# Kernel tuning notes

Hardware: AMD Instinct MI355X
Metric: run time of the kernel (lower is better)

The kernel has to match this reference:

```python
import jax, jax.numpy as jnp
import numpy as np

B, L, S = 1, 2048, 2048
D_MODEL, H = 1024, 16
DK = D_MODEL // H  # d_keys = d_values = 64


def sparsemax(z):
    # sparsemax along last axis: proj of z onto the simplex
    K = z.shape[-1]
    z_sorted = jnp.flip(jnp.sort(z, axis=-1), axis=-1)
    cs = jnp.cumsum(z_sorted, axis=-1)
    r = jnp.arange(1, K + 1, dtype=z.dtype)
    support = 1.0 + r * z_sorted > cs
    k = jnp.sum(support, axis=-1, keepdims=True)
    tau = (jnp.take_along_axis(cs, k.astype(jnp.int32) - 1, axis=-1) - 1.0) / k.astype(z.dtype)
    return jnp.maximum(z - tau, 0.0)


def setup_inputs() -> dict:
    key = jax.random.key(0)
    ks = jax.random.split(key, 12)
    sc = 1.0 / np.sqrt(D_MODEL)
    return {
        "queries": jax.random.normal(ks[0], (B, L, D_MODEL), jnp.float32),
        "keys": jax.random.normal(ks[1], (B, S, D_MODEL), jnp.float32),
        "values": jax.random.normal(ks[2], (B, S, D_MODEL), jnp.float32),
        "Wq": jax.random.normal(ks[3], (D_MODEL, H * DK), jnp.float32) * sc,
        "bq": jnp.zeros((H * DK,), jnp.float32),
        "Wk": jax.random.normal(ks[4], (D_MODEL, H * DK), jnp.float32) * sc,
        "bk": jnp.zeros((H * DK,), jnp.float32),
        "Wv": jax.random.normal(ks[5], (H * DK, H * DK), jnp.float32) * sc,
        "bv": jnp.zeros((H * DK,), jnp.float32),
        "Wo": jax.random.normal(ks[6], (H * DK, D_MODEL), jnp.float32) * sc,
        "bo": jnp.zeros((D_MODEL,), jnp.float32),
    }


def reference(queries, keys, values, Wq, bq, Wk, bk, Wv, bv, Wo, bo):
    # projections (note: input `values` is unused, matching the torch source)
    q = (queries @ Wq + bq).reshape(B, L, H, DK)
    k_flat = keys @ Wk + bk                      # [B,S,H*DK]
    k = k_flat.reshape(B, S, H, DK)
    v = (k_flat @ Wv + bv).reshape(B, S, H, DK)  # value_projection(key_projection(keys))
    scale = 1.0 / np.sqrt(DK)
    scores = jnp.einsum('blhe,bshe->bhls', q, k) * scale  # [B,H,L,S]
    A = sparsemax(scores)
    out = jnp.einsum('bhls,bshd->blhd', A, v)             # [B,L,H,DK]
    # mix=True: transpose(2,1) -> [B,H,L,D] then view(B,L,-1)
    out = jnp.swapaxes(out, 1, 2).reshape(B, L, H * DK)
    return out @ Wo + bo
```

## Files before the change

### kernel.cpp

```cpp
#include <hip/hip_runtime.h>
#include <hip/hip_bf16.h>


typedef __attribute__((ext_vector_type(8))) short short8;
typedef __attribute__((ext_vector_type(4))) float floatx4;

#define SRC_BF16 0
#define SRC_F32  1
#define SRC_RT   2
#define CAP 128

__device__ __forceinline__ short f2bf(float f) {
    __hip_bfloat16 h = __float2bfloat16(f);
    return *reinterpret_cast<const short*>(&h);
}
__device__ __forceinline__ unsigned short f2bfu(float f) {
    __hip_bfloat16 h = __float2bfloat16(f);
    return *reinterpret_cast<const unsigned short*>(&h);
}
__device__ __forceinline__ float bf2f(unsigned short u) {
    return __uint_as_float(((unsigned)u) << 16);
}
__device__ __forceinline__ unsigned fmap(float f) {
    unsigned u = __float_as_uint(f);
    return (u & 0x80000000u) ? ~u : (u | 0x80000000u);
}
__device__ __forceinline__ float funmap(unsigned u) {
    return (u & 0x80000000u) ? __uint_as_float(u ^ 0x80000000u) : __uint_as_float(~u);
}

__global__ void detect_k(const short* __restrict__ q, int n, int* __restrict__ flag)
{
    const int tid = threadIdx.x;
    int bad = 0;
    for (int i = tid; i < n; i += 64) {
        float f = bf2f((unsigned short)q[i]);
        if (!(fabsf(f) < 1e10f)) bad = 1;
    }
    unsigned long long m = __ballot(bad != 0);
    if (tid == 0) *flag = (m != 0ULL) ? 1 : 0;
}

__global__ __launch_bounds__(256)
void convert2_k(const void* __restrict__ s0, const void* __restrict__ s1,
                short* __restrict__ d0, short* __restrict__ d1,
                const int* __restrict__ dflag)
{
    const void* s = blockIdx.z ? s1 : s0;
    short* d = blockIdx.z ? d1 : d0;
    const size_t i = ((size_t)blockIdx.x * 256 + threadIdx.x) * 8;
    short8 o;
    if (*dflag) {
        const float4 f0 = ((const float4*)((const float*)s + i))[0];
        const float4 f1 = ((const float4*)((const float*)s + i))[1];
        o[0] = f2bf(f0.x); o[1] = f2bf(f0.y); o[2] = f2bf(f0.z); o[3] = f2bf(f0.w);
        o[4] = f2bf(f1.x); o[5] = f2bf(f1.y); o[6] = f2bf(f1.z); o[7] = f2bf(f1.w);
    } else {
        o = *(const short8*)((const short*)s + i);
    }
    *(short8*)(d + i) = o;
}

struct TP4 {
    const void* s[4];
    short* d[4];
};
__global__ __launch_bounds__(256)
void transpose4_k(TP4 p, int R, int C, const int* __restrict__ dflag)
{
    __shared__ short T[64][72];
    const int tid = threadIdx.x;
    const int bC = blockIdx.x, bR = blockIdx.y;
    const void* src = p.s[blockIdx.z];
    short* dst = p.d[blockIdx.z];
    const bool f32 = (*dflag != 0);

    const int colg = (tid & 7) * 8;
    #pragma unroll
    for (int h = 0; h < 2; ++h) {
        const int row = (tid >> 3) + 32 * h;
        const size_t idx = (size_t)(bR * 64 + row) * (size_t)C + (size_t)(bC * 64 + colg);
        short e[8];
        if (f32) {
            const float4 f0 = ((const float4*)((const float*)src + idx))[0];
            const float4 f1 = ((const float4*)((const float*)src + idx))[1];
            e[0] = f2bf(f0.x); e[1] = f2bf(f0.y); e[2] = f2bf(f0.z); e[3] = f2bf(f0.w);
            e[4] = f2bf(f1.x); e[5] = f2bf(f1.y); e[6] = f2bf(f1.z); e[7] = f2bf(f1.w);
        } else {
            short8 s = *(const short8*)((const short*)src + idx);
            #pragma unroll
            for (int j = 0; j < 8; ++j) e[j] = s[j];
        }
        #pragma unroll
        for (int j = 0; j < 8; ++j) T[colg + j][row] = e[j];
    }
    __syncthreads();
    #pragma unroll
    for (int h = 0; h < 2; ++h) {
        const int orow = (tid >> 3) + 32 * h;
        const int ocolg = (tid & 7) * 8;
        const size_t idx = (size_t)(bC * 64 + orow) * (size_t)R + (size_t)(bR * 64 + ocolg);
        *(short8*)(dst + idx) = *(const short8*)&T[orow][ocolg];
    }
}

struct GJ { const short* A; const short* B; const void* bias; void* C; };

template<int OSRC>
__global__ __launch_bounds__(256)
void gemm64_bt_k(GJ j0, GJ j1, const int* __restrict__ dflag)
{
    __shared__ __align__(16) short As[64][40];
    __shared__ __align__(16) short Bs[64][40];

    const GJ j = blockIdx.z ? j1 : j0;
    const int rtf = *dflag;

    const int tid  = threadIdx.x;
    const int bN   = blockIdx.x, bM = blockIdx.y;
    const int lane = tid & 63, wave = tid >> 6;
    const int wm   = (wave >> 1) * 32;
    const int wn   = (wave & 1) * 32;
    const int quad = lane >> 4, r16 = lane & 15;

    floatx4 acc[2][2];
    #pragma unroll
    for (int i = 0; i < 2; ++i)
        #pragma unroll
        for (int jj = 0; jj < 2; ++jj)
            acc[i][jj] = (floatx4){0.f, 0.f, 0.f, 0.f};

    const int ar = tid >> 2, ac = (tid & 3) * 8;

    for (int k0 = 0; k0 < 1024; k0 += 32) {
        *(short8*)&As[ar][ac] =
            *(const short8*)(j.A + (size_t)(bM * 64 + ar) * 1024 + (size_t)(k0 + ac));
        *(short8*)&Bs[ar][ac] =
            *(const short8*)(j.B + (size_t)(bN * 64 + ar) * 1024 + (size_t)(k0 + ac));
        __syncthreads();

        short8 a0 = *(const short8*)&As[wm + r16][quad * 8];
        short8 a1 = *(const short8*)&As[wm + 16 + r16][quad * 8];
        short8 b0 = *(const short8*)&Bs[wn + r16][quad * 8];
        short8 b1 = *(const short8*)&Bs[wn + 16 + r16][quad * 8];

        acc[0][0] = __builtin_amdgcn_mfma_f32_16x16x32_bf16(a0, b0, acc[0][0], 0, 0, 0);
        acc[0][1] = __builtin_amdgcn_mfma_f32_16x16x32_bf16(a0, b1, acc[0][1], 0, 0, 0);
        acc[1][0] = __builtin_amdgcn_mfma_f32_16x16x32_bf16(a1, b0, acc[1][0], 0, 0, 0);
        acc[1][1] = __builtin_amdgcn_mfma_f32_16x16x32_bf16(a1, b1, acc[1][1], 0, 0, 0);
        __syncthreads();
    }

    const bool of32 = (OSRC == SRC_F32) || (OSRC == SRC_RT && rtf);
    #pragma unroll
    for (int jj = 0; jj < 2; ++jj) {
        const int gc = bN * 64 + wn + jj * 16 + r16;
        const float bb = rtf ? ((const float*)j.bias)[gc]
                             : bf2f(((const unsigned short*)j.bias)[gc]);
        #pragma unroll
        for (int i = 0; i < 2; ++i) {
            #pragma unroll
            for (int rg = 0; rg < 4; ++rg) {
                const int gr = bM * 64 + wm + i * 16 + quad * 4 + rg;
                const float v = acc[i][jj][rg] + bb;
                if (of32)
                    ((float*)j.C)[(size_t)gr * 1024 + gc] = v;
                else
                    ((__hip_bfloat16*)j.C)[(size_t)gr * 1024 + gc] = __float2bfloat16(v);
            }
        }
    }
}

__global__ __launch_bounds__(256, 4)
void attn_fused_k(const short* __restrict__ Qb, const short* __restrict__ Kb,
                  const short* __restrict__ Vb, short* __restrict__ Ob)
{
    __shared__ __align__(16) short sQ[32][72];
    __shared__ __align__(16) short sK[128][72];
    __shared__ unsigned cpk[32][CAP];
    __shared__ unsigned rmax[32];
    __shared__ int cnt[32];

    const int tid  = threadIdx.x;
    const int lane = tid & 63, wave = tid >> 6;
    const int quad = lane >> 4, r16 = lane & 15;
    const int row0 = blockIdx.x * 32;
    const int h    = blockIdx.y;
    const int sp   = (wave >> 1) * 16;
    const int hf   = wave & 1;
    const int myrow = sp + quad * 4;

    if (tid < 32) { rmax[tid] = 0u; cnt[tid] = 0; }
    {
        const int r = tid >> 3, c = (tid & 7) * 8;
        *(short8*)&sQ[r][c] = *(const short8*)(Qb + (size_t)(row0 + r) * 1024 + h * 64 + c);
    }
    __syncthreads();

    const short8 qa0 = *(const short8*)&sQ[sp + r16][quad * 8];
    const short8 qa1 = *(const short8*)&sQ[sp + r16][32 + quad * 8];

    float rm1[4], rm2[4];
    #pragma unroll
    for (int rg = 0; rg < 4; ++rg) { rm1[rg] = -3.0e38f; rm2[rg] = -3.0e38f; }

    for (int s0 = 0; s0 < 2048; s0 += 128) {
        #pragma unroll
        for (int i = 0; i < 4; ++i) {
            const int kr = (tid >> 3) + 32 * i, c = (tid & 7) * 8;
            *(short8*)&sK[kr][c] = *(const short8*)(Kb + (size_t)(s0 + kr) * 1024 + h * 64 + c);
        }
        __syncthreads();

        floatx4 acc[4];
        #pragma unroll
        for (int t = 0; t < 4; ++t) {
            const int ct = (hf + 2 * t) * 16;
            const short8 b0 = *(const short8*)&sK[ct + r16][quad * 8];
            const short8 b1 = *(const short8*)&sK[ct + r16][32 + quad * 8];
            floatx4 a = (floatx4){0.f, 0.f, 0.f, 0.f};
            a = __builtin_amdgcn_mfma_f32_16x16x32_bf16(qa0, b0, a, 0, 0, 0);
            a = __builtin_amdgcn_mfma_f32_16x16x32_bf16(qa1, b1, a, 0, 0, 0);
            #pragma unroll
            for (int rg = 0; rg < 4; ++rg) a[rg] *= 0.125f;
            acc[t] = a;
        }

        #pragma unroll
        for (int rg = 0; rg < 4; ++rg) {
            float m1ab = fmaxf(acc[0][rg], acc[1][rg]);
            float m2ab = fminf(acc[0][rg], acc[1][rg]);
            float m1cd = fmaxf(acc[2][rg], acc[3][rg]);
            float m2cd = fminf(acc[2][rg], acc[3][rg]);
            float m1 = fmaxf(m1ab, m1cd);
            float m2 = fmaxf(fminf(m1ab, m1cd), (m1ab >= m1cd) ? m2ab : m2cd);
            #pragma unroll
            for (int off = 1; off < 16; off <<= 1) {
                const float o1 = __shfl_xor(m1, off, 64);
                const float o2 = __shfl_xor(m2, off, 64);
                const float n2 = fmaxf(fminf(m1, o1), (m1 >= o1) ? m2 : o2);
                m1 = fmaxf(m1, o1);
                m2 = n2;
            }
            const float n1 = fmaxf(rm1[rg], m1);
            rm2[rg] = fmaxf(fminf(rm1[rg], m1), (rm1[rg] >= m1) ? rm2[rg] : m2);
            rm1[rg] = n1;
            if (r16 == 0) atomicMax(&rmax[myrow + rg], fmap(m1));
        }
        __syncthreads();

        #pragma unroll
        for (int rg = 0; rg < 4; ++rg) {
            const int row = myrow + rg;
            const float g1 = funmap(rmax[row]);
            const float thr = fmaxf(g1 - 1.0f, 0.5f * (g1 + rm2[rg]) - 0.5f);
            #pragma unroll
            for (int t = 0; t < 4; ++t) {
                const float val = acc[t][rg];
                const bool keep = (val >= thr);
                const unsigned long long m = __ballot(keep);
                const unsigned qm = (unsigned)((m >> (quad * 16)) & 0xFFFFull);
                int base = 0;
                if (r16 == 0 && qm) base = atomicAdd(&cnt[row], __popc(qm));
                base = __shfl(base, quad * 16, 64);
                if (keep) {
                    const int p = base + __popc(qm & ((1u << r16) - 1u));
                    if (p < CAP)
                        cpk[row][p] = ((unsigned)f2bfu(val) << 16)
                                    | (unsigned)(s0 + (hf + 2 * t) * 16 + r16);
                }
            }
        }
    }
    __syncthreads();

    const unsigned long long pre = (1ULL << lane) - 1ULL;
    for (int rr = 0; rr < 8; ++rr) {
        const int r = wave * 8 + rr;
        const int n = min(cnt[r], CAP);

        float v[2];
        unsigned short ii[2];
        #pragma unroll
        for (int i = 0; i < 2; ++i) {
            const int ix = lane + i * 64;
            if (ix < n) {
                const unsigned u = cpk[r][ix];
                v[i] = bf2f((unsigned short)(u >> 16));
                ii[i] = (unsigned short)(u & 0xFFFFu);
            } else { v[i] = -3.0e38f; ii[i] = 0; }
        }

        float tau = -3.0e38f, prevc = -1.0f;
        for (int it = 0; it < 24; ++it) {
            float s = 0.f, c = 0.f;
            #pragma unroll
            for (int i = 0; i < 2; ++i)
                if (v[i] > tau) { s += v[i]; c += 1.f; }
            #pragma unroll
            for (int off = 1; off < 64; off <<= 1) {
                s += __shfl_xor(s, off, 64);
                c += __shfl_xor(c, off, 64);
            }
            if (c == prevc) break;
            prevc = c;
            tau = (s - 1.0f) / c;
        }

        int base = 0;
        #pragma unroll
        for (int i = 0; i < 2; ++i) {
            const float p = v[i] - tau;
            const unsigned long long m = __ballot(p > 0.f);
            const int w = base + __popcll(m & pre);
            if (p > 0.f) cpk[r][w] = ((unsigned)f2bfu(p) << 16) | (unsigned)ii[i];
            base += __popcll(m);
        }
        const int msup = base;

        const unsigned short* vb = (const unsigned short*)Vb + (size_t)h * 64 + lane;
        float o0 = 0.f, o1 = 0.f, o2 = 0.f, o3 = 0.f;
        int jj = 0;
        for (; jj + 4 <= msup; jj += 4) {
            const unsigned u0 = cpk[r][jj],     u1 = cpk[r][jj + 1];
            const unsigned u2 = cpk[r][jj + 2], u3 = cpk[r][jj + 3];
            o0 += bf2f((unsigned short)(u0 >> 16)) * bf2f(vb[(size_t)(u0 & 0xFFFFu) * 1024]);
            o1 += bf2f((unsigned short)(u1 >> 16)) * bf2f(vb[(size_t)(u1 & 0xFFFFu) * 1024]);
            o2 += bf2f((unsigned short)(u2 >> 16)) * bf2f(vb[(size_t)(u2 & 0xFFFFu) * 1024]);
            o3 += bf2f((unsigned short)(u3 >> 16)) * bf2f(vb[(size_t)(u3 & 0xFFFFu) * 1024]);
        }
        for (; jj < msup; ++jj) {
            const unsigned u0 = cpk[r][jj];
            o0 += bf2f((unsigned short)(u0 >> 16)) * bf2f(vb[(size_t)(u0 & 0xFFFFu) * 1024]);
        }
        Ob[((size_t)h * 2048 + row0 + r) * 64 + lane] = f2bf(o0 + o1 + o2 + o3);
    }
}

extern "C" void kernel_launch(void* const* d_in, const int* in_sizes, int n_in,
                              void* d_out, int out_size, void* d_ws, size_t ws_size,
                              hipStream_t stream)
{
    (void)in_sizes; (void)n_in; (void)out_size; (void)ws_size;

    const void* queries = d_in[0];
    const void* keys    = d_in[1];
    const void* Wq = d_in[3];
    const void* bq = d_in[4];
    const void* Wk = d_in[5];
    const void* bk = d_in[6];
    const void* Wv = d_in[7];
    const void* bv = d_in[8];
    const void* Wo = d_in[9];
    const void* bo = d_in[10];

    const int L = 2048, DM = 1024;
    const size_t LD = (size_t)L * DM;

    int*   flag = (int*)d_ws;
    short* Qc  = (short*)((char*)d_ws + 256);
    short* Kc  = Qc + LD;
    short* WqT = Kc + LD;
    short* WkT = WqT + (size_t)DM * DM;
    short* WvT = WkT + (size_t)DM * DM;
    short* WoT = WvT + (size_t)DM * DM;
    short* Qb  = WoT + (size_t)DM * DM;
    short* Kb  = Qb + LD;
    short* Vb  = Kb + LD;
    short* Ob  = Vb + LD;

    dim3 blk(256);

    detect_k<<<dim3(1), dim3(64), 0, stream>>>((const short*)queries, 4096, flag);

    convert2_k<<<dim3((unsigned)(LD / 2048), 1, 2), blk, 0, stream>>>(
        queries, keys, Qc, Kc, flag);

    {
        TP4 p;
        p.s[0] = Wq; p.s[1] = Wk; p.s[2] = Wv; p.s[3] = Wo;
        p.d[0] = WqT; p.d[1] = WkT; p.d[2] = WvT; p.d[3] = WoT;
        transpose4_k<<<dim3(DM / 64, DM / 64, 4), blk, 0, stream>>>(p, DM, DM, flag);
    }

    {
        GJ jq{(const short*)Qc, WqT, bq, Qb};
        GJ jk{(const short*)Kc, WkT, bk, Kb};
        gemm64_bt_k<SRC_BF16><<<dim3(DM / 64, L / 64, 2), blk, 0, stream>>>(jq, jk, flag);
    }
    {
        GJ jv{(const short*)Kb, WvT, bv, Vb};
        gemm64_bt_k<SRC_BF16><<<dim3(DM / 64, L / 64, 1), blk, 0, stream>>>(jv, jv, flag);
    }

    attn_fused_k<<<dim3(L / 32, 16), blk, 0, stream>>>(Qb, Kb, Vb, Ob);

    {
        GJ jo{(const short*)Ob, WoT, bo, d_out};
        gemm64_bt_k<SRC_RT><<<dim3(DM / 64, L / 64, 1), blk, 0, stream>>>(jo, jo, flag);
    }
}
```

Measured before the change: 271.7 us.

## Restructure sparse attention to 16-row blocks with direct global K loads

The attention kernel now handles 16 query rows per block instead of 32, and each wave covers a different slice of keys for the same rows. Q and K fragments are loaded straight from global memory into registers, so the shared-memory staging and the per-tile barriers are gone. The candidate threshold now uses the running block max merged with the wave's local max, which allows it to proceed without a barrier. Block ids are remapped so that neighbouring blocks share rows across heads, CAP grows to 192, and launch bounds are raised to 8 blocks per CU. In exchange there are more uncoalesced global loads, and the threshold can be looser, which may admit more candidates.

```diff
diff --git a/kernel.cpp b/kernel.cpp
--- a/kernel.cpp
+++ b/kernel.cpp
@@ -8,7 +8,7 @@
 #define SRC_BF16 0
 #define SRC_F32  1
 #define SRC_RT   2
-#define CAP 128
+#define CAP 192
 
 __device__ __forceinline__ short f2bf(float f) {
     __hip_bfloat16 h = __float2bfloat16(f);
@@ -172,53 +172,44 @@
     }
 }
 
-__global__ __launch_bounds__(256, 4)
+__global__ __launch_bounds__(256, 8)
 void attn_fused_k(const short* __restrict__ Qb, const short* __restrict__ Kb,
                   const short* __restrict__ Vb, short* __restrict__ Ob)
 {
-    __shared__ __align__(16) short sQ[32][72];
-    __shared__ __align__(16) short sK[128][72];
-    __shared__ unsigned cpk[32][CAP];
-    __shared__ unsigned rmax[32];
-    __shared__ int cnt[32];
+    __shared__ unsigned cpk[16][CAP];
+    __shared__ unsigned rmax[16];
+    __shared__ int cnt[16];
 
     const int tid  = threadIdx.x;
     const int lane = tid & 63, wave = tid >> 6;
     const int quad = lane >> 4, r16 = lane & 15;
-    const int row0 = blockIdx.x * 32;
-    const int h    = blockIdx.y;
-    const int sp   = (wave >> 1) * 16;
-    const int hf   = wave & 1;
-    const int myrow = sp + quad * 4;
-
-    if (tid < 32) { rmax[tid] = 0u; cnt[tid] = 0; }
-    {
-        const int r = tid >> 3, c = (tid & 7) * 8;
-        *(short8*)&sQ[r][c] = *(const short8*)(Qb + (size_t)(row0 + r) * 1024 + h * 64 + c);
-    }
+
+    const int bid  = blockIdx.x;
+    const int slot = bid >> 3;
+    const int h    = (slot & 1) * 8 + (bid & 7);
+    const int row0 = (slot >> 1) * 16;
+
+    if (tid < 16) { rmax[tid] = fmap(-3.0e38f); cnt[tid] = 0; }
     __syncthreads();
 
-    const short8 qa0 = *(const short8*)&sQ[sp + r16][quad * 8];
-    const short8 qa1 = *(const short8*)&sQ[sp + r16][32 + quad * 8];
+    const short* qp = Qb + (size_t)(row0 + r16) * 1024 + h * 64 + quad * 8;
+    const short8 qa0 = *(const short8*)qp;
+    const short8 qa1 = *(const short8*)(qp + 32);
+
+    const int myrow = quad * 4;
+    const short* kp0 = Kb + (size_t)(wave * 16 + r16) * 1024 + h * 64 + quad * 8;
 
     float rm1[4], rm2[4];
     #pragma unroll
     for (int rg = 0; rg < 4; ++rg) { rm1[rg] = -3.0e38f; rm2[rg] = -3.0e38f; }
 
-    for (int s0 = 0; s0 < 2048; s0 += 128) {
-        #pragma unroll
-        for (int i = 0; i < 4; ++i) {
-            const int kr = (tid >> 3) + 32 * i, c = (tid & 7) * 8;
-            *(short8*)&sK[kr][c] = *(const short8*)(Kb + (size_t)(s0 + kr) * 1024 + h * 64 + c);
-        }
-        __syncthreads();
-
+    for (int s0 = 0; s0 < 2048; s0 += 256) {
         floatx4 acc[4];
         #pragma unroll
         for (int t = 0; t < 4; ++t) {
-            const int ct = (hf + 2 * t) * 16;
-            const short8 b0 = *(const short8*)&sK[ct + r16][quad * 8];
-            const short8 b1 = *(const short8*)&sK[ct + r16][32 + quad * 8];
+            const short* kp = kp0 + (size_t)(s0 + t * 64) * 1024;
+            const short8 b0 = *(const short8*)kp;
+            const short8 b1 = *(const short8*)(kp + 32);
             floatx4 a = (floatx4){0.f, 0.f, 0.f, 0.f};
             a = __builtin_amdgcn_mfma_f32_16x16x32_bf16(qa0, b0, a, 0, 0, 0);
             a = __builtin_amdgcn_mfma_f32_16x16x32_bf16(qa1, b1, a, 0, 0, 0);
@@ -248,12 +239,11 @@
             rm1[rg] = n1;
             if (r16 == 0) atomicMax(&rmax[myrow + rg], fmap(m1));
         }
-        __syncthreads();
 
         #pragma unroll
         for (int rg = 0; rg < 4; ++rg) {
             const int row = myrow + rg;
-            const float g1 = funmap(rmax[row]);
+            const float g1 = fmaxf(funmap(rmax[row]), rm1[rg]);
             const float thr = fmaxf(g1 - 1.0f, 0.5f * (g1 + rm2[rg]) - 0.5f);
             #pragma unroll
             for (int t = 0; t < 4; ++t) {
@@ -268,7 +258,7 @@
                     const int p = base + __popc(qm & ((1u << r16) - 1u));
                     if (p < CAP)
                         cpk[row][p] = ((unsigned)f2bfu(val) << 16)
-                                    | (unsigned)(s0 + (hf + 2 * t) * 16 + r16);
+                                    | (unsigned)(s0 + wave * 16 + t * 64 + r16);
                 }
             }
         }
@@ -276,14 +266,14 @@
     __syncthreads();
 
     const unsigned long long pre = (1ULL << lane) - 1ULL;
-    for (int rr = 0; rr < 8; ++rr) {
-        const int r = wave * 8 + rr;
+    for (int rr = 0; rr < 4; ++rr) {
+        const int r = wave * 4 + rr;
         const int n = min(cnt[r], CAP);
 
-        float v[2];
-        unsigned short ii[2];
-        #pragma unroll
-        for (int i = 0; i < 2; ++i) {
+        float v[3];
+        unsigned short ii[3];
+        #pragma unroll
+        for (int i = 0; i < 3; ++i) {
             const int ix = lane + i * 64;
             if (ix < n) {
                 const unsigned u = cpk[r][ix];
@@ -296,7 +286,7 @@
         for (int it = 0; it < 24; ++it) {
             float s = 0.f, c = 0.f;
             #pragma unroll
-            for (int i = 0; i < 2; ++i)
+            for (int i = 0; i < 3; ++i)
                 if (v[i] > tau) { s += v[i]; c += 1.f; }
             #pragma unroll
             for (int off = 1; off < 64; off <<= 1) {
@@ -310,7 +300,7 @@
 
         int base = 0;
         #pragma unroll
-        for (int i = 0; i < 2; ++i) {
+        for (int i = 0; i < 3; ++i) {
             const float p = v[i] - tau;
             const unsigned long long m = __ballot(p > 0.f);
             const int w = base + __popcll(m & pre);
@@ -394,7 +384,7 @@
         gemm64_bt_k<SRC_BF16><<<dim3(DM / 64, L / 64, 1), blk, 0, stream>>>(jv, jv, flag);
     }
 
-    attn_fused_k<<<dim3(L / 32, 16), blk, 0, stream>>>(Qb, Kb, Vb, Ob);
+    attn_fused_k<<<dim3((L / 16) * 16), blk, 0, stream>>>(Qb, Kb, Vb, Ob);
 
     {
         GJ jo{(const short*)Ob, WoT, bo, d_out};
```

Result: no change. 266.4 us (-1.9%).
